# Kernel tuning notes

Measured on AMD Instinct MI355X. Metric: run time of the kernel, lower is better.

## Reference

```python
import jax, jax.numpy as jnp
import numpy as np
import math

B, T, H = 2, 1024, 2048
NH, NKV, HD = 8, 2, 256
S = 4           # altup_num_inputs
FF = 8192       # intermediate_size
LR = 64         # laurel_rank
EPS = 1e-6
ROPE_THETA = 1e6


def _ln(x, w):
    # Gemma3nRMSNorm in this repo: fp32 mean-subtract then F.layer_norm (no bias)
    x32 = x.astype(jnp.float32)
    xc = x32 - x32.mean(-1, keepdims=True)
    var = (xc * xc).mean(-1, keepdims=True)
    return (xc * jax.lax.rsqrt(var + EPS) * w.astype(jnp.float32)).astype(x.dtype)


def _rotate_half(x):
    x1, x2 = jnp.split(x, 2, axis=-1)
    return jnp.concatenate((-x2, x1), axis=-1)


def _rope(x, cos, sin):  # x: [B,nh,T,hd]; cos/sin: [B,T,hd]
    return x * cos[:, None] + _rotate_half(x) * sin[:, None]


def setup_inputs() -> dict:
    key = jax.random.key(0)
    ks = jax.random.split(key, 24)

    def w(k, shape, scale=0.02):
        return jax.random.normal(k, shape, jnp.float32) * scale

    hidden_states = jax.random.normal(ks[0], (S, B, T, H), jnp.float32)

    # real rotary embeddings
    inv_freq = 1.0 / (ROPE_THETA ** (np.arange(0, HD, 2, dtype=np.float64) / HD))
    freqs = np.arange(T, dtype=np.float64)[:, None] * inv_freq[None, :]
    emb = np.concatenate([freqs, freqs], axis=-1)  # [T,HD]
    cos = jnp.broadcast_to(jnp.asarray(np.cos(emb), jnp.float32)[None], (B, T, HD))
    sin = jnp.broadcast_to(jnp.asarray(np.sin(emb), jnp.float32)[None], (B, T, HD))

    return {
        "hidden_states": hidden_states, "cos": cos, "sin": sin,
        "wq": w(ks[1], (NH * HD, H)), "wk": w(ks[2], (NKV * HD, H)),
        "wv": w(ks[3], (NKV * HD, H)), "wo": w(ks[4], (H, NH * HD)),
        "q_norm_w": jnp.ones((HD,), jnp.float32), "k_norm_w": jnp.ones((HD,), jnp.float32),
        "input_ln_w": jnp.ones((H,), jnp.float32), "post_attn_ln_w": jnp.ones((H,), jnp.float32),
        "pre_ffw_ln_w": jnp.ones((H,), jnp.float32), "post_ffw_ln_w": jnp.ones((H,), jnp.float32),
        "gate_w": w(ks[5], (FF, H)), "up_w": w(ks[6], (FF, H)), "down_w": w(ks[7], (H, FF)),
        "laurel_left_w": w(ks[8], (LR, H)), "laurel_right_w": w(ks[9], (H, LR)),
        "laurel_norm_w": jnp.ones((H,), jnp.float32),
        "router_norm_w": jnp.ones((H,), jnp.float32),
        "router_w": w(ks[10], (S, H)),
        "pred_coef_w": w(ks[11], (S * S, S)),
        "corr_coef_w": w(ks[12], (S, S)),
        "correct_output_scale": w(ks[13], (H,), 1.0),
    }


def reference(hidden_states, cos, sin, wq, wk, wv, wo, q_norm_w, k_norm_w,
              input_ln_w, post_attn_ln_w, pre_ffw_ln_w, post_ffw_ln_w,
              gate_w, up_w, down_w, laurel_left_w, laurel_right_w, laurel_norm_w,
              router_norm_w, router_w, pred_coef_w, corr_coef_w, correct_output_scale):
    def modalities_of(x):  # router: RMSNorm -> scale -> linear -> tanh
        r = _ln(x, router_norm_w) * (1.0 / H)
        return jnp.tanh((r @ router_w.T).astype(jnp.float32)).astype(x.dtype)

    # ---- AltUp predict ----
    m = modalities_of(hidden_states[0])                      # [B,T,S]
    coefs = (m @ pred_coef_w.T).reshape(B, T, S, S)          # raw [B,T,S_out,S_in]
    # torch: matmul(h.permute(1,2,3,0), coefs.permute(0,1,3,2)) => sum_s h[s]*raw[...,j,s]
    predictions = jnp.einsum('sbth,btjs->jbth', hidden_states, coefs) + hidden_states

    active = predictions[0]
    x_norm = _ln(active, input_ln_w)

    # ---- Laurel block ----
    lau = (x_norm @ laurel_left_w.T) @ laurel_right_w.T
    laurel_out = x_norm + _ln(lau, laurel_norm_w)

    # ---- Attention (GQA, q/k/v norms, rope, scale=1.0) ----
    q = _ln((x_norm @ wq.T).reshape(B, T, NH, HD), q_norm_w).transpose(0, 2, 1, 3)
    q = _rope(q, cos, sin)
    k = _ln((x_norm @ wk.T).reshape(B, T, NKV, HD), k_norm_w).transpose(0, 2, 1, 3)
    k = _rope(k, cos, sin)
    v = _ln((x_norm @ wv.T).reshape(B, T, NKV, HD), jnp.ones((HD,), jnp.float32))
    v = v.transpose(0, 2, 1, 3)
    rep = NH // NKV
    k = jnp.repeat(k, rep, axis=1)
    v = jnp.repeat(v, rep, axis=1)
    scores = jnp.einsum('bhqd,bhkd->bhqk', q, k)             # scaling = 1.0 in Gemma3n
    causal = jnp.tril(jnp.ones((T, T), bool))
    scores = jnp.where(causal, scores, jnp.finfo(jnp.float32).min)
    attn = jax.nn.softmax(scores.astype(jnp.float32), axis=-1).astype(q.dtype)
    out = jnp.einsum('bhqk,bhkd->bhqd', attn, v)
    out = out.transpose(0, 2, 1, 3).reshape(B, T, NH * HD) @ wo.T
    out = _ln(out, post_attn_ln_w)

    attn_gated = active + out
    attn_laurel = (attn_gated + laurel_out) * (1.0 / math.sqrt(2.0))

    # ---- MLP (gelu-tanh gated) ----
    h = _ln(attn_laurel, pre_ffw_ln_w)
    ffw = (jax.nn.gelu(h @ gate_w.T, approximate=True) * (h @ up_w.T)) @ down_w.T
    ffw = _ln(ffw, post_ffw_ln_w)
    activated = attn_laurel + ffw

    # ---- AltUp correct ----
    mc = modalities_of(activated)                            # [B,T,S]
    innovation = activated - predictions[0]                  # [B,T,H]
    ccoefs = (mc @ corr_coef_w.T) + 1.0                      # [B,T,S]
    corrected = innovation[None] * ccoefs.transpose(2, 0, 1)[..., None] + predictions

    # scale_corrected_output on the active stream (altup_correct_scale=True)
    first = (corrected[0] * correct_output_scale).astype(corrected.dtype)
    corrected = corrected.at[0].set(first)
    return corrected
```

## Files before the change

kernel.cpp:

```cpp
#include <hip/hip_runtime.h>
#include <hip/hip_bf16.h>
#include <math.h>

#define B_   2
#define T_   1024
#define H_   2048
#define NH_  8
#define NKV_ 2
#define HD_  256
#define S_   4
#define FF_  8192
#define LR_  64
#define ROWS_ (B_*T_)
#define EPS_ 1e-6f

typedef __attribute__((ext_vector_type(8))) __bf16 bf16x8;
typedef __attribute__((ext_vector_type(4))) float floatx4;
typedef __attribute__((ext_vector_type(8))) unsigned short ushort8v;

__device__ __forceinline__ unsigned short f2bf(float f) {
    unsigned int u = __float_as_uint(f);
    return (unsigned short)((u + 0x7FFFu + ((u >> 16) & 1u)) >> 16);
}

__device__ __forceinline__ void gl_lds16(const void* g, void* l) {
    __builtin_amdgcn_global_load_lds(
        (const __attribute__((address_space(1))) void*)g,
        (__attribute__((address_space(3))) void*)l, 16, 0, 0);
}

__device__ __forceinline__ int swz_sigma(int r15) {
    return (r15 & 3) ^ ((r15 >> 2) & 3);
}

__device__ __forceinline__ float block_sum(float v) {
    __shared__ float s4[4];
    #pragma unroll
    for (int o = 32; o > 0; o >>= 1) v += __shfl_down(v, o, 64);
    int lane = threadIdx.x & 63;
    int w    = threadIdx.x >> 6;
    __syncthreads();
    if (lane == 0) s4[w] = v;
    __syncthreads();
    return s4[0] + s4[1] + s4[2] + s4[3];
}

__device__ __forceinline__ float block_max(float v) {
    __shared__ float s4m[4];
    #pragma unroll
    for (int o = 32; o > 0; o >>= 1) v = fmaxf(v, __shfl_down(v, o, 64));
    int lane = threadIdx.x & 63;
    int w    = threadIdx.x >> 6;
    __syncthreads();
    if (lane == 0) s4m[w] = v;
    __syncthreads();
    return fmaxf(fmaxf(s4m[0], s4m[1]), fmaxf(s4m[2], s4m[3]));
}

__global__ __launch_bounds__(256) void cvt_bf16(
    const float* __restrict__ in, unsigned short* __restrict__ out, int n)
{
    int i = (blockIdx.x * 256 + threadIdx.x) * 8;
    if (i >= n) return;
    float4 v0 = *reinterpret_cast<const float4*>(in + i);
    float4 v1 = *reinterpret_cast<const float4*>(in + i + 4);
    ushort8v o;
    o[0] = f2bf(v0.x); o[1] = f2bf(v0.y); o[2] = f2bf(v0.z); o[3] = f2bf(v0.w);
    o[4] = f2bf(v1.x); o[5] = f2bf(v1.y); o[6] = f2bf(v1.z); o[7] = f2bf(v1.w);
    *reinterpret_cast<ushort8v*>(out + i) = o;
}

__global__ __launch_bounds__(256) void router_kernel(
    const float* __restrict__ x, const float* __restrict__ nw,
    const float* __restrict__ rw, float* __restrict__ mout)
{
    size_t row = blockIdx.x;
    int tid = threadIdx.x;
    const float* xr = x + row * H_;
    float v[8]; float s = 0.f;
    #pragma unroll
    for (int i = 0; i < 8; ++i) { v[i] = xr[i*256 + tid]; s += v[i]; }
    float mu = block_sum(s) * (1.f / H_);
    float ss = 0.f;
    #pragma unroll
    for (int i = 0; i < 8; ++i) { float c = v[i] - mu; ss += c * c; }
    float rstd = rsqrtf(block_sum(ss) * (1.f / H_) + EPS_);
    float n[8];
    #pragma unroll
    for (int i = 0; i < 8; ++i) n[i] = (v[i] - mu) * rstd * nw[i*256 + tid];
    for (int so = 0; so < S_; ++so) {
        float p = 0.f;
        #pragma unroll
        for (int i = 0; i < 8; ++i) p += n[i] * rw[(size_t)so * H_ + i*256 + tid];
        float dot = block_sum(p);
        if (tid == 0) mout[row * S_ + so] = tanhf(dot * (1.f / H_));
    }
}

__global__ __launch_bounds__(256) void predict_kernel(
    const float* __restrict__ hid, const float* __restrict__ m,
    const float* __restrict__ pcw, float* __restrict__ pred)
{
    size_t row = blockIdx.x;
    int tid = threadIdx.x;
    __shared__ float ms[4];
    __shared__ float c[16];
    if (tid < 4) ms[tid] = m[row * S_ + tid];
    __syncthreads();
    if (tid < 16) {
        float s = 0.f;
        #pragma unroll
        for (int i = 0; i < 4; ++i) s += ms[i] * pcw[tid * 4 + i];
        c[tid] = s;
    }
    __syncthreads();
    const size_t STRIDE = (size_t)ROWS_ * H_;
    #pragma unroll
    for (int i = 0; i < 8; ++i) {
        size_t idx = row * H_ + i*256 + tid;
        float h0 = hid[idx];
        float h1 = hid[idx + STRIDE];
        float h2 = hid[idx + 2*STRIDE];
        float h3 = hid[idx + 3*STRIDE];
        float hv[4] = {h0, h1, h2, h3};
        #pragma unroll
        for (int j = 0; j < 4; ++j) {
            float val = hv[j] + h0*c[j*4+0] + h1*c[j*4+1] + h2*c[j*4+2] + h3*c[j*4+3];
            pred[idx + (size_t)j * STRIDE] = val;
        }
    }
}

__global__ __launch_bounds__(256) void ln_residual(
    const float* __restrict__ x, const float* __restrict__ xadd,
    const float* __restrict__ w,
    const float* __restrict__ a1, const float* __restrict__ a2,
    float scale, float* __restrict__ out, unsigned short* __restrict__ outb)
{
    size_t row = blockIdx.x;
    int tid = threadIdx.x;
    const float* xr = x + row * H_;
    const float* xa = xadd ? xadd + row * H_ : nullptr;
    float v[8]; float s = 0.f;
    #pragma unroll
    for (int i = 0; i < 8; ++i) {
        v[i] = xr[i*256 + tid];
        if (xa) v[i] += xa[i*256 + tid];
        s += v[i];
    }
    float mu = block_sum(s) * (1.f / H_);
    float ss = 0.f;
    #pragma unroll
    for (int i = 0; i < 8; ++i) { float c = v[i] - mu; ss += c * c; }
    float rstd = rsqrtf(block_sum(ss) * (1.f / H_) + EPS_);
    #pragma unroll
    for (int i = 0; i < 8; ++i) {
        size_t idx = row * H_ + i*256 + tid;
        float y = (v[i] - mu) * rstd * w[i*256 + tid];
        if (a1) y += a1[idx];
        if (a2) y += a2[idx];
        y *= scale;
        if (out)  out[idx]  = y;
        if (outb) outb[idx] = f2bf(y);
    }
}

#define BM 64
#define BN 64
#define BK 32
#define LDP 68

__global__ __launch_bounds__(256) void gemm_nt(
    const float* __restrict__ A, const float* __restrict__ Bm,
    float* __restrict__ C, int M, int N, int K)
{
    __shared__ float As[BK][LDP];
    __shared__ float Bs[BK][LDP];
    int tid = threadIdx.x;
    int n0 = blockIdx.x * BN;
    int m0 = blockIdx.y * BM;
    int tx = tid & 15, ty = tid >> 4;
    int lrow = tid >> 3;
    int lk   = (tid & 7) << 2;
    float acc[4][4] = {};
    for (int k0 = 0; k0 < K; k0 += BK) {
        #pragma unroll
        for (int r = 0; r < 2; ++r) {
            int row = lrow + r * 32;
            float4 a4 = *reinterpret_cast<const float4*>(&A[(size_t)(m0 + row) * K + k0 + lk]);
            As[lk+0][row] = a4.x; As[lk+1][row] = a4.y; As[lk+2][row] = a4.z; As[lk+3][row] = a4.w;
            float4 b4 = *reinterpret_cast<const float4*>(&Bm[(size_t)(n0 + row) * K + k0 + lk]);
            Bs[lk+0][row] = b4.x; Bs[lk+1][row] = b4.y; Bs[lk+2][row] = b4.z; Bs[lk+3][row] = b4.w;
        }
        __syncthreads();
        #pragma unroll
        for (int k = 0; k < BK; ++k) {
            float4 av = *reinterpret_cast<const float4*>(&As[k][ty << 2]);
            float4 bv = *reinterpret_cast<const float4*>(&Bs[k][tx << 2]);
            float a[4] = {av.x, av.y, av.z, av.w};
            float b[4] = {bv.x, bv.y, bv.z, bv.w};
            #pragma unroll
            for (int i = 0; i < 4; ++i)
                #pragma unroll
                for (int j = 0; j < 4; ++j)
                    acc[i][j] = fmaf(a[i], b[j], acc[i][j]);
        }
        __syncthreads();
    }
    #pragma unroll
    for (int i = 0; i < 4; ++i) {
        float4 o; o.x = acc[i][0]; o.y = acc[i][1]; o.z = acc[i][2]; o.w = acc[i][3];
        *reinterpret_cast<float4*>(&C[(size_t)(m0 + (ty << 2) + i) * N + n0 + (tx << 2)]) = o;
    }
}

__global__ __launch_bounds__(256) void gemm_bf16nt(
    const unsigned short* __restrict__ A, const unsigned short* __restrict__ Bm,
    float* __restrict__ C, float* __restrict__ C2, int M, int N, int K)
{
    __shared__ unsigned short As[8192];
    __shared__ unsigned short Bs[8192];
    int tid = threadIdx.x;
    int lane = tid & 63;
    int wave = tid >> 6;
    int m0 = blockIdx.y * 128, n0 = blockIdx.x * 128;
    int Kper = K / gridDim.z;
    int kbeg = blockIdx.z * Kper;
    int kend = kbeg + Kper;
    int wm = (wave >> 1) * 64;
    int wn = (wave & 1) * 64;
    floatx4 acc[4][4] = {};

    int lr = lane >> 2;
    int kcs = (lane & 3) ^ swz_sigma(lr);
    const unsigned short* aG0 = A  + (size_t)(m0 + wave*16 + lr) * K + kcs * 8;
    const unsigned short* aG1 = aG0 + (size_t)64 * K;
    const unsigned short* bG0 = Bm + (size_t)(n0 + wave*16 + lr) * K + kcs * 8;
    const unsigned short* bG1 = bG0 + (size_t)64 * K;

    int kc = lane >> 4, mr = lane & 15;
    int kcp = (kc ^ swz_sigma(mr)) * 8;

    gl_lds16(aG0 + kbeg, &As[wave * 512]);
    gl_lds16(aG1 + kbeg, &As[2048 + wave * 512]);
    gl_lds16(bG0 + kbeg, &Bs[wave * 512]);
    gl_lds16(bG1 + kbeg, &Bs[2048 + wave * 512]);
    __syncthreads();
    int cur = 0;
    for (int k0 = kbeg; k0 < kend; k0 += 32) {
        if (k0 + 32 < kend) {
            int nb = (cur ^ 1) * 4096;
            gl_lds16(aG0 + k0 + 32, &As[nb + wave * 512]);
            gl_lds16(aG1 + k0 + 32, &As[nb + 2048 + wave * 512]);
            gl_lds16(bG0 + k0 + 32, &Bs[nb + wave * 512]);
            gl_lds16(bG1 + k0 + 32, &Bs[nb + 2048 + wave * 512]);
        }
        int cb = cur * 4096;
        bf16x8 af[4], bfv[4];
        #pragma unroll
        for (int mi = 0; mi < 4; ++mi)
            af[mi] = *reinterpret_cast<const bf16x8*>(&As[cb + (wm + mi * 16 + mr) * 32 + kcp]);
        #pragma unroll
        for (int ni = 0; ni < 4; ++ni)
            bfv[ni] = *reinterpret_cast<const bf16x8*>(&Bs[cb + (wn + ni * 16 + mr) * 32 + kcp]);
        #pragma unroll
        for (int mi = 0; mi < 4; ++mi)
            #pragma unroll
            for (int ni = 0; ni < 4; ++ni)
                acc[mi][ni] = __builtin_amdgcn_mfma_f32_16x16x32_bf16(af[mi], bfv[ni], acc[mi][ni], 0, 0, 0);
        __syncthreads();
        cur ^= 1;
    }
    float* Cout = (blockIdx.z == 0) ? C : C2;
    int quad = lane >> 4;
    #pragma unroll
    for (int mi = 0; mi < 4; ++mi)
        #pragma unroll
        for (int ni = 0; ni < 4; ++ni)
            #pragma unroll
            for (int r = 0; r < 4; ++r)
                Cout[(size_t)(m0 + wm + mi * 16 + quad * 4 + r) * N + n0 + wn + ni * 16 + mr] = acc[mi][ni][r];
}

__global__ __launch_bounds__(256) void gemm_gateup_bf16(
    const unsigned short* __restrict__ A, const unsigned short* __restrict__ G,
    const unsigned short* __restrict__ U, unsigned short* __restrict__ Cbf,
    int M, int N, int K)
{
    __shared__ unsigned short As[8192];
    __shared__ unsigned short Gs[8192];
    __shared__ unsigned short Us[8192];
    int tid = threadIdx.x;
    int lane = tid & 63;
    int wave = tid >> 6;
    int m0 = blockIdx.y * 128, n0 = blockIdx.x * 128;
    int wm  = (wave >> 1) * 64;
    int wnf = (wave & 1) * 64;
    floatx4 accg[4][4] = {};
    floatx4 accu[4][4] = {};

    int lr = lane >> 2;
    int kcs = (lane & 3) ^ swz_sigma(lr);
    const unsigned short* aG0 = A + (size_t)(m0 + wave*16 + lr) * K + kcs * 8;
    const unsigned short* aG1 = aG0 + (size_t)64 * K;
    const unsigned short* gG0 = G + (size_t)(n0 + wave*16 + lr) * K + kcs * 8;
    const unsigned short* gG1 = gG0 + (size_t)64 * K;
    const unsigned short* uG0 = U + (size_t)(n0 + wave*16 + lr) * K + kcs * 8;
    const unsigned short* uG1 = uG0 + (size_t)64 * K;

    int kc = lane >> 4, mr = lane & 15;
    int kcp = (kc ^ swz_sigma(mr)) * 8;

    gl_lds16(aG0, &As[wave * 512]);
    gl_lds16(aG1, &As[2048 + wave * 512]);
    gl_lds16(gG0, &Gs[wave * 512]);
    gl_lds16(gG1, &Gs[2048 + wave * 512]);
    gl_lds16(uG0, &Us[wave * 512]);
    gl_lds16(uG1, &Us[2048 + wave * 512]);
    __syncthreads();
    int cur = 0;
    for (int k0 = 0; k0 < K; k0 += 32) {
        if (k0 + 32 < K) {
            int nb = (cur ^ 1) * 4096;
            gl_lds16(aG0 + k0 + 32, &As[nb + wave * 512]);
            gl_lds16(aG1 + k0 + 32, &As[nb + 2048 + wave * 512]);
            gl_lds16(gG0 + k0 + 32, &Gs[nb + wave * 512]);
            gl_lds16(gG1 + k0 + 32, &Gs[nb + 2048 + wave * 512]);
            gl_lds16(uG0 + k0 + 32, &Us[nb + wave * 512]);
            gl_lds16(uG1 + k0 + 32, &Us[nb + 2048 + wave * 512]);
        }
        int cb = cur * 4096;
        bf16x8 af[4], gf[4], uf[4];
        #pragma unroll
        for (int mi = 0; mi < 4; ++mi)
            af[mi] = *reinterpret_cast<const bf16x8*>(&As[cb + (wm + mi * 16 + mr) * 32 + kcp]);
        #pragma unroll
        for (int ni = 0; ni < 4; ++ni) {
            gf[ni] = *reinterpret_cast<const bf16x8*>(&Gs[cb + (wnf + ni * 16 + mr) * 32 + kcp]);
            uf[ni] = *reinterpret_cast<const bf16x8*>(&Us[cb + (wnf + ni * 16 + mr) * 32 + kcp]);
        }
        #pragma unroll
        for (int mi = 0; mi < 4; ++mi)
            #pragma unroll
            for (int ni = 0; ni < 4; ++ni) {
                accg[mi][ni] = __builtin_amdgcn_mfma_f32_16x16x32_bf16(af[mi], gf[ni], accg[mi][ni], 0, 0, 0);
                accu[mi][ni] = __builtin_amdgcn_mfma_f32_16x16x32_bf16(af[mi], uf[ni], accu[mi][ni], 0, 0, 0);
            }
        __syncthreads();
        cur ^= 1;
    }
    int quad = lane >> 4;
    #pragma unroll
    for (int mi = 0; mi < 4; ++mi) {
        int rb = m0 + wm + mi * 16 + quad * 4;
        #pragma unroll
        for (int ni = 0; ni < 4; ++ni)
            #pragma unroll
            for (int r = 0; r < 4; ++r) {
                float g = accg[mi][ni][r];
                float gl = 0.5f * g * (1.f + tanhf(0.7978845608028654f * (g + 0.044715f * g * g * g)));
                float val = gl * accu[mi][ni][r];
                Cbf[(size_t)(rb + r) * N + n0 + wnf + ni * 16 + mr] = f2bf(val);
            }
    }
}

__global__ __launch_bounds__(256) void qkv_norm_rope_fused(
    const float* __restrict__ in, const float* __restrict__ qw,
    const float* __restrict__ kw,
    const float* __restrict__ cs, const float* __restrict__ sn,
    unsigned short* __restrict__ qo, unsigned short* __restrict__ ko,
    unsigned short* __restrict__ vo)
{
    int blk = blockIdx.x;
    int hh = blk % 12;
    int trow = blk / 12;
    int b = trow / T_;
    int t = trow % T_;
    int d = threadIdx.x;
    float x = in[(size_t)trow * 3072 + hh * HD_ + d];
    float mu = block_sum(x) * (1.f / HD_);
    float xc = x - mu;
    float var = block_sum(xc * xc) * (1.f / HD_);
    float wv_ = (hh < 8) ? qw[d] : (hh < 10 ? kw[d] : 1.f);
    float n = xc * rsqrtf(var + EPS_) * wv_;
    __shared__ float buf[HD_];
    buf[d] = n;
    __syncthreads();
    float val = n;
    if (hh < 10) {
        float c = cs[(size_t)trow * HD_ + d];
        float s = sn[(size_t)trow * HD_ + d];
        float other = (d < 128) ? -buf[d + 128] : buf[d - 128];
        val = n * c + other * s;
    }
    if (hh < 8)
        qo[(((size_t)b * NH_ + hh) * T_ + t) * HD_ + d] = f2bf(val);
    else if (hh < 10)
        ko[(((size_t)b * NKV_ + (hh - 8)) * T_ + t) * HD_ + d] = f2bf(val);
    else
        vo[(((size_t)b * NKV_ + (hh - 10)) * HD_ + d) * T_ + t] = f2bf(val);
}

__global__ __launch_bounds__(256) void qk_gemm(
    const unsigned short* __restrict__ Q, const unsigned short* __restrict__ Kt,
    float* __restrict__ S, int head_base)
{
    if (blockIdx.x > blockIdx.y) return;
    int z = blockIdx.z;
    int bh = head_base + z;
    const unsigned short* A  = Q  + (size_t)bh * T_ * HD_;
    const unsigned short* Bm = Kt + (size_t)(bh >> 2) * T_ * HD_;
    float* C = S + (size_t)z * T_ * T_;

    __shared__ unsigned short As[8192];
    __shared__ unsigned short Bs[8192];
    int tid = threadIdx.x;
    int lane = tid & 63;
    int wave = tid >> 6;
    int m0 = blockIdx.y * 128, n0 = blockIdx.x * 128;
    int wm = (wave >> 1) * 64;
    int wn = (wave & 1) * 64;
    floatx4 acc[4][4] = {};

    int lr = lane >> 2;
    int kcs = (lane & 3) ^ swz_sigma(lr);
    const unsigned short* aG0 = A  + (size_t)(m0 + wave*16 + lr) * HD_ + kcs * 8;
    const unsigned short* aG1 = aG0 + (size_t)64 * HD_;
    const unsigned short* bG0 = Bm + (size_t)(n0 + wave*16 + lr) * HD_ + kcs * 8;
    const unsigned short* bG1 = bG0 + (size_t)64 * HD_;

    int kc = lane >> 4, mr = lane & 15;
    int kcp = (kc ^ swz_sigma(mr)) * 8;

    gl_lds16(aG0, &As[wave * 512]);
    gl_lds16(aG1, &As[2048 + wave * 512]);
    gl_lds16(bG0, &Bs[wave * 512]);
    gl_lds16(bG1, &Bs[2048 + wave * 512]);
    __syncthreads();
    int cur = 0;
    for (int k0 = 0; k0 < HD_; k0 += 32) {
        if (k0 + 32 < HD_) {
            int nb = (cur ^ 1) * 4096;
            gl_lds16(aG0 + k0 + 32, &As[nb + wave * 512]);
            gl_lds16(aG1 + k0 + 32, &As[nb + 2048 + wave * 512]);
            gl_lds16(bG0 + k0 + 32, &Bs[nb + wave * 512]);
            gl_lds16(bG1 + k0 + 32, &Bs[nb + 2048 + wave * 512]);
        }
        int cb = cur * 4096;
        bf16x8 af[4], bfv[4];
        #pragma unroll
        for (int mi = 0; mi < 4; ++mi)
            af[mi] = *reinterpret_cast<const bf16x8*>(&As[cb + (wm + mi * 16 + mr) * 32 + kcp]);
        #pragma unroll
        for (int ni = 0; ni < 4; ++ni)
            bfv[ni] = *reinterpret_cast<const bf16x8*>(&Bs[cb + (wn + ni * 16 + mr) * 32 + kcp]);
        #pragma unroll
        for (int mi = 0; mi < 4; ++mi)
            #pragma unroll
            for (int ni = 0; ni < 4; ++ni)
                acc[mi][ni] = __builtin_amdgcn_mfma_f32_16x16x32_bf16(af[mi], bfv[ni], acc[mi][ni], 0, 0, 0);
        __syncthreads();
        cur ^= 1;
    }
    int quad = lane >> 4;
    #pragma unroll
    for (int mi = 0; mi < 4; ++mi)
        #pragma unroll
        for (int ni = 0; ni < 4; ++ni)
            #pragma unroll
            for (int r = 0; r < 4; ++r)
                C[(size_t)(m0 + wm + mi * 16 + quad * 4 + r) * T_ + n0 + wn + ni * 16 + mr] = acc[mi][ni][r];
}

__global__ __launch_bounds__(256) void softmax_causal(
    const float* __restrict__ S, unsigned short* __restrict__ P)
{
    int qi = blockIdx.x;
    int g  = blockIdx.y;
    int tid = threadIdx.x;
    int L = qi + 1;
    const float* Srow = S + ((size_t)g * T_ + qi) * T_;
    unsigned short* Prow = P + ((size_t)g * T_ + qi) * T_;
    float v[4];
    float mx = -3.402823466e38f;
    #pragma unroll
    for (int i = 0; i < 4; ++i) {
        int idx = i * 256 + tid;
        v[i] = (idx < L) ? Srow[idx] : -3.402823466e38f;
        mx = fmaxf(mx, v[i]);
    }
    mx = block_max(mx);
    float sm = 0.f;
    float e[4];
    #pragma unroll
    for (int i = 0; i < 4; ++i) {
        int idx = i * 256 + tid;
        e[i] = (idx < L) ? expf(v[i] - mx) : 0.f;
        sm += e[i];
    }
    sm = block_sum(sm);
    float inv = 1.f / sm;
    #pragma unroll
    for (int i = 0; i < 4; ++i)
        Prow[i * 256 + tid] = f2bf(e[i] * inv);
}

__global__ __launch_bounds__(256) void pv_gemm(
    const unsigned short* __restrict__ P, const unsigned short* __restrict__ Vt,
    unsigned short* __restrict__ Out)
{
    int z = blockIdx.z;
    int b = z >> 3;
    int h = z & 7;
    const unsigned short* A  = P  + (size_t)z * T_ * T_;
    const unsigned short* Bm = Vt + (size_t)(z >> 2) * HD_ * T_;

    __shared__ unsigned short As[8192];
    __shared__ unsigned short Bs[8192];
    int tid = threadIdx.x;
    int lane = tid & 63;
    int wave = tid >> 6;
    int m0 = blockIdx.y * 128, n0 = blockIdx.x * 128;
    int Kend = m0 + 128;
    int wm = (wave >> 1) * 64;
    int wn = (wave & 1) * 64;
    floatx4 acc[4][4] = {};

    int lr = lane >> 2;
    int kcs = (lane & 3) ^ swz_sigma(lr);
    const unsigned short* aG0 = A  + (size_t)(m0 + wave*16 + lr) * T_ + kcs * 8;
    const unsigned short* aG1 = aG0 + (size_t)64 * T_;
    const unsigned short* bG0 = Bm + (size_t)(n0 + wave*16 + lr) * T_ + kcs * 8;
    const unsigned short* bG1 = bG0 + (size_t)64 * T_;

    int kc = lane >> 4, mr = lane & 15;
    int kcp = (kc ^ swz_sigma(mr)) * 8;

    gl_lds16(aG0, &As[wave * 512]);
    gl_lds16(aG1, &As[2048 + wave * 512]);
    gl_lds16(bG0, &Bs[wave * 512]);
    gl_lds16(bG1, &Bs[2048 + wave * 512]);
    __syncthreads();
    int cur = 0;
    for (int k0 = 0; k0 < Kend; k0 += 32) {
        if (k0 + 32 < Kend) {
            int nb = (cur ^ 1) * 4096;
            gl_lds16(aG0 + k0 + 32, &As[nb + wave * 512]);
            gl_lds16(aG1 + k0 + 32, &As[nb + 2048 + wave * 512]);
            gl_lds16(bG0 + k0 + 32, &Bs[nb + wave * 512]);
            gl_lds16(bG1 + k0 + 32, &Bs[nb + 2048 + wave * 512]);
        }
        int cb = cur * 4096;
        bf16x8 af[4], bfv[4];
        #pragma unroll
        for (int mi = 0; mi < 4; ++mi)
            af[mi] = *reinterpret_cast<const bf16x8*>(&As[cb + (wm + mi * 16 + mr) * 32 + kcp]);
        #pragma unroll
        for (int ni = 0; ni < 4; ++ni)
            bfv[ni] = *reinterpret_cast<const bf16x8*>(&Bs[cb + (wn + ni * 16 + mr) * 32 + kcp]);
        #pragma unroll
        for (int mi = 0; mi < 4; ++mi)
            #pragma unroll
            for (int ni = 0; ni < 4; ++ni)
                acc[mi][ni] = __builtin_amdgcn_mfma_f32_16x16x32_bf16(af[mi], bfv[ni], acc[mi][ni], 0, 0, 0);
        __syncthreads();
        cur ^= 1;
    }
    int quad = lane >> 4;
    #pragma unroll
    for (int mi = 0; mi < 4; ++mi)
        #pragma unroll
        for (int ni = 0; ni < 4; ++ni)
            #pragma unroll
            for (int r = 0; r < 4; ++r) {
                int row = m0 + wm + mi * 16 + quad * 4 + r;
                int col = n0 + wn + ni * 16 + mr;
                Out[((size_t)(b * T_ + row)) * (NH_ * HD_) + h * HD_ + col] =
                    f2bf(acc[mi][ni][r]);
            }
}

__global__ __launch_bounds__(256) void correct_kernel(
    const float* __restrict__ act, const float* __restrict__ pred,
    const float* __restrict__ mc, const float* __restrict__ ccw,
    const float* __restrict__ cscale, float* __restrict__ out)
{
    size_t row = blockIdx.x;
    int tid = threadIdx.x;
    __shared__ float ms[4];
    __shared__ float cc[4];
    if (tid < 4) ms[tid] = mc[row * S_ + tid];
    __syncthreads();
    if (tid < 4) {
        float s = 1.f;
        #pragma unroll
        for (int i = 0; i < 4; ++i) s += ms[i] * ccw[tid * 4 + i];
        cc[tid] = s;
    }
    __syncthreads();
    const size_t STRIDE = (size_t)ROWS_ * H_;
    #pragma unroll
    for (int i = 0; i < 8; ++i) {
        size_t idx = row * H_ + i*256 + tid;
        float a  = act[idx];
        float p0 = pred[idx];
        float inn = a - p0;
        #pragma unroll
        for (int j = 0; j < 4; ++j) {
            float val = inn * cc[j] + pred[idx + (size_t)j * STRIDE];
            if (j == 0) val *= cscale[i*256 + tid];
            out[idx + (size_t)j * STRIDE] = val;
        }
    }
}

extern "C" void kernel_launch(void* const* d_in, const int* in_sizes, int n_in,
                              void* d_out, int out_size, void* d_ws, size_t ws_size,
                              hipStream_t stream)
{
    (void)in_sizes; (void)n_in; (void)out_size; (void)ws_size;
    const float* hidden         = (const float*)d_in[0];
    const float* cosp           = (const float*)d_in[1];
    const float* sinp           = (const float*)d_in[2];
    const float* wq             = (const float*)d_in[3];
    const float* wk             = (const float*)d_in[4];
    const float* wv             = (const float*)d_in[5];
    const float* wo             = (const float*)d_in[6];
    const float* q_norm_w       = (const float*)d_in[7];
    const float* k_norm_w       = (const float*)d_in[8];
    const float* input_ln_w     = (const float*)d_in[9];
    const float* post_attn_ln_w = (const float*)d_in[10];
    const float* pre_ffw_ln_w   = (const float*)d_in[11];
    const float* post_ffw_ln_w  = (const float*)d_in[12];
    const float* gate_w         = (const float*)d_in[13];
    const float* up_w           = (const float*)d_in[14];
    const float* down_w         = (const float*)d_in[15];
    const float* ll_w           = (const float*)d_in[16];
    const float* lr_w           = (const float*)d_in[17];
    const float* laurel_norm_w  = (const float*)d_in[18];
    const float* router_norm_w  = (const float*)d_in[19];
    const float* router_w       = (const float*)d_in[20];
    const float* pred_coef_w    = (const float*)d_in[21];
    const float* corr_coef_w    = (const float*)d_in[22];
    const float* cscale         = (const float*)d_in[23];
    float* outp = (float*)d_out;

    char* base = (char*)d_ws;
    float* pred   = (float*)base;              base += 67108864;
    float* xnorm  = (float*)base;              base += 16777216;
    unsigned short* xnorm_bf = (unsigned short*)base; base += 8388608;
    float* lout   = (float*)base;              base += 16777216;
    float* alaur  = (float*)base;              base += 16777216;
    float* tmpH   = (float*)base;              base += 16777216;
    float* mbuf   = (float*)base;              base += 32768;
    float* mcbuf  = (float*)base;              base += 32768;
    float* ltmp   = (float*)base;              base += 524288;
    char* arena = base;
    unsigned short* qkvw_bf = (unsigned short*)arena;
    float* qkv_pre = (float*)(arena + 12582912);
    unsigned short* Pbuf    = (unsigned short*)arena;
    unsigned short* q_bf    = (unsigned short*)(arena + 37748736);
    unsigned short* k_bf    = (unsigned short*)(arena + 46137344);
    unsigned short* vT_bf   = (unsigned short*)(arena + 48234496);
    unsigned short* attn_bf = (unsigned short*)(arena + 50331648);
    unsigned short* wo_bf   = (unsigned short*)(arena + 58720256);
    float* Sbuf             = (float*)(arena + 67108864);
    unsigned short* gate_bf = (unsigned short*)arena;
    unsigned short* up_bf   = (unsigned short*)(arena + 33554432);
    unsigned short* gu_bf   = (unsigned short*)(arena + 67108864);
    unsigned short* down_bf = gate_bf;
    float* activated = lout;

    router_kernel <<<ROWS_, 256, 0, stream>>>(hidden, router_norm_w, router_w, mbuf);
    predict_kernel<<<ROWS_, 256, 0, stream>>>(hidden, mbuf, pred_coef_w, pred);
    ln_residual   <<<ROWS_, 256, 0, stream>>>(pred, nullptr, input_ln_w, nullptr, nullptr, 1.f, xnorm, xnorm_bf);

    gemm_nt<<<dim3(LR_/BN, ROWS_/BM), 256, 0, stream>>>(xnorm, ll_w, ltmp, ROWS_, LR_, H_);
    gemm_nt<<<dim3(H_/BN,  ROWS_/BM), 256, 0, stream>>>(ltmp, lr_w, tmpH, ROWS_, H_, LR_);
    ln_residual<<<ROWS_, 256, 0, stream>>>(tmpH, nullptr, laurel_norm_w, xnorm, nullptr, 1.f, lout, nullptr);

    cvt_bf16<<<2048, 256, 0, stream>>>(wq, qkvw_bf,            4194304);
    cvt_bf16<<< 512, 256, 0, stream>>>(wk, qkvw_bf + 4194304,  1048576);
    cvt_bf16<<< 512, 256, 0, stream>>>(wv, qkvw_bf + 5242880,  1048576);
    gemm_bf16nt<<<dim3(24, 16, 1), 256, 0, stream>>>(xnorm_bf, qkvw_bf, qkv_pre, nullptr, ROWS_, 3072, H_);
    qkv_norm_rope_fused<<<ROWS_*12, 256, 0, stream>>>(qkv_pre, q_norm_w, k_norm_w, cosp, sinp, q_bf, k_bf, vT_bf);
    cvt_bf16<<<2048, 256, 0, stream>>>(wo, wo_bf, 4194304);
    for (int hb = 0; hb < B_ * NH_; hb += 8) {
        qk_gemm       <<<dim3(8, 8, 8), 256, 0, stream>>>(q_bf, k_bf, Sbuf, hb);
        softmax_causal<<<dim3(T_, 8),   256, 0, stream>>>(Sbuf, Pbuf + (size_t)hb * T_ * T_);
    }
    pv_gemm<<<dim3(2, 8, 16), 256, 0, stream>>>(Pbuf, vT_bf, attn_bf);
    gemm_bf16nt<<<dim3(16, 16, 2), 256, 0, stream>>>(attn_bf, wo_bf, tmpH, xnorm, ROWS_, H_, NH_*HD_);
    ln_residual<<<ROWS_, 256, 0, stream>>>(tmpH, xnorm, post_attn_ln_w, pred, lout, 0.7071067811865475f, alaur, nullptr);

    ln_residual<<<ROWS_, 256, 0, stream>>>(alaur, nullptr, pre_ffw_ln_w, nullptr, nullptr, 1.f, nullptr, xnorm_bf);
    cvt_bf16<<<8192, 256, 0, stream>>>(gate_w, gate_bf, 16777216);
    cvt_bf16<<<8192, 256, 0, stream>>>(up_w,   up_bf,   16777216);
    gemm_gateup_bf16<<<dim3(64, 16), 256, 0, stream>>>(xnorm_bf, gate_bf, up_bf, gu_bf, ROWS_, FF_, H_);
    cvt_bf16<<<8192, 256, 0, stream>>>(down_w, down_bf, 16777216);
    gemm_bf16nt<<<dim3(16, 16, 2), 256, 0, stream>>>(gu_bf, down_bf, tmpH, xnorm, ROWS_, H_, FF_);
    ln_residual<<<ROWS_, 256, 0, stream>>>(tmpH, xnorm, post_ffw_ln_w, alaur, nullptr, 1.f, activated, nullptr);

    router_kernel <<<ROWS_, 256, 0, stream>>>(activated, router_norm_w, router_w, mcbuf);
    correct_kernel<<<ROWS_, 256, 0, stream>>>(activated, pred, mcbuf, corr_coef_w, cscale, outp);
}
```

Baseline: 1.114 ms.

## Rework gate/up GEMM to 128x64 tiles with register-staged single-buffer LDS

Rewrites the fused gate/up GEMM kernel to use 128x64 output tiles instead of 128x128, with each wave computing 32 rows across all 64 columns. The global-to-LDS async loads with a double buffer are replaced by register prefetch into a single LDS buffer with two barriers per k-step, using a k-chunk-major LDS layout without the XOR swizzle. The grid doubles to keep coverage. The aim is lower LDS and register use for higher occupancy, at the cost of less operand reuse per block and extra synchronisation.

Result: faster. 1.020 ms (-8.4%).

```diff
diff --git a/kernel.cpp b/kernel.cpp
--- a/kernel.cpp
+++ b/kernel.cpp
@@ -287,72 +287,67 @@
     const unsigned short* __restrict__ U, unsigned short* __restrict__ Cbf,
     int M, int N, int K)
 {
-    __shared__ unsigned short As[8192];
-    __shared__ unsigned short Gs[8192];
-    __shared__ unsigned short Us[8192];
+    __shared__ unsigned short As[4096];
+    __shared__ unsigned short Gs[2048];
+    __shared__ unsigned short Us[2048];
     int tid = threadIdx.x;
     int lane = tid & 63;
     int wave = tid >> 6;
-    int m0 = blockIdx.y * 128, n0 = blockIdx.x * 128;
-    int wm  = (wave >> 1) * 64;
-    int wnf = (wave & 1) * 64;
-    floatx4 accg[4][4] = {};
-    floatx4 accu[4][4] = {};
-
-    int lr = lane >> 2;
-    int kcs = (lane & 3) ^ swz_sigma(lr);
-    const unsigned short* aG0 = A + (size_t)(m0 + wave*16 + lr) * K + kcs * 8;
-    const unsigned short* aG1 = aG0 + (size_t)64 * K;
-    const unsigned short* gG0 = G + (size_t)(n0 + wave*16 + lr) * K + kcs * 8;
-    const unsigned short* gG1 = gG0 + (size_t)64 * K;
-    const unsigned short* uG0 = U + (size_t)(n0 + wave*16 + lr) * K + kcs * 8;
-    const unsigned short* uG1 = uG0 + (size_t)64 * K;
+    int m0 = blockIdx.y * 128, n0 = blockIdx.x * 64;
+    floatx4 accg[2][4] = {};
+    floatx4 accu[2][4] = {};
+
+    int cm = tid >> 2;
+    int ck = tid & 3;
+    const unsigned short* aP0 = A + (size_t)(m0 + cm)      * K + ck * 8;
+    const unsigned short* aP1 = A + (size_t)(m0 + 64 + cm) * K + ck * 8;
+    const unsigned short* gP  = G + (size_t)(n0 + cm)      * K + ck * 8;
+    const unsigned short* uP  = U + (size_t)(n0 + cm)      * K + ck * 8;
+    unsigned short* aW0 = &As[(ck * 128 + cm) * 8];
+    unsigned short* aW1 = &As[(ck * 128 + 64 + cm) * 8];
+    unsigned short* gW  = &Gs[(ck * 64 + cm) * 8];
+    unsigned short* uW  = &Us[(ck * 64 + cm) * 8];
+
+    uint4 ra0 = *reinterpret_cast<const uint4*>(aP0);
+    uint4 ra1 = *reinterpret_cast<const uint4*>(aP1);
+    uint4 rg  = *reinterpret_cast<const uint4*>(gP);
+    uint4 ru  = *reinterpret_cast<const uint4*>(uP);
 
     int kc = lane >> 4, mr = lane & 15;
-    int kcp = (kc ^ swz_sigma(mr)) * 8;
-
-    gl_lds16(aG0, &As[wave * 512]);
-    gl_lds16(aG1, &As[2048 + wave * 512]);
-    gl_lds16(gG0, &Gs[wave * 512]);
-    gl_lds16(gG1, &Gs[2048 + wave * 512]);
-    gl_lds16(uG0, &Us[wave * 512]);
-    gl_lds16(uG1, &Us[2048 + wave * 512]);
-    __syncthreads();
-    int cur = 0;
     for (int k0 = 0; k0 < K; k0 += 32) {
+        __syncthreads();
+        *reinterpret_cast<uint4*>(aW0) = ra0;
+        *reinterpret_cast<uint4*>(aW1) = ra1;
+        *reinterpret_cast<uint4*>(gW)  = rg;
+        *reinterpret_cast<uint4*>(uW)  = ru;
+        __syncthreads();
         if (k0 + 32 < K) {
-            int nb = (cur ^ 1) * 4096;
-            gl_lds16(aG0 + k0 + 32, &As[nb + wave * 512]);
-            gl_lds16(aG1 + k0 + 32, &As[nb + 2048 + wave * 512]);
-            gl_lds16(gG0 + k0 + 32, &Gs[nb + wave * 512]);
-            gl_lds16(gG1 + k0 + 32, &Gs[nb + 2048 + wave * 512]);
-            gl_lds16(uG0 + k0 + 32, &Us[nb + wave * 512]);
-            gl_lds16(uG1 + k0 + 32, &Us[nb + 2048 + wave * 512]);
-        }
-        int cb = cur * 4096;
-        bf16x8 af[4], gf[4], uf[4];
-        #pragma unroll
-        for (int mi = 0; mi < 4; ++mi)
-            af[mi] = *reinterpret_cast<const bf16x8*>(&As[cb + (wm + mi * 16 + mr) * 32 + kcp]);
+            ra0 = *reinterpret_cast<const uint4*>(aP0 + k0 + 32);
+            ra1 = *reinterpret_cast<const uint4*>(aP1 + k0 + 32);
+            rg  = *reinterpret_cast<const uint4*>(gP + k0 + 32);
+            ru  = *reinterpret_cast<const uint4*>(uP + k0 + 32);
+        }
+        bf16x8 af[2], gf[4], uf[4];
+        #pragma unroll
+        for (int mi = 0; mi < 2; ++mi)
+            af[mi] = *reinterpret_cast<const bf16x8*>(&As[kc * 1024 + (wave * 32 + mi * 16 + mr) * 8]);
         #pragma unroll
         for (int ni = 0; ni < 4; ++ni) {
-            gf[ni] = *reinterpret_cast<const bf16x8*>(&Gs[cb + (wnf + ni * 16 + mr) * 32 + kcp]);
-            uf[ni] = *reinterpret_cast<const bf16x8*>(&Us[cb + (wnf + ni * 16 + mr) * 32 + kcp]);
-        }
-        #pragma unroll
-        for (int mi = 0; mi < 4; ++mi)
+            gf[ni] = *reinterpret_cast<const bf16x8*>(&Gs[kc * 512 + (ni * 16 + mr) * 8]);
+            uf[ni] = *reinterpret_cast<const bf16x8*>(&Us[kc * 512 + (ni * 16 + mr) * 8]);
+        }
+        #pragma unroll
+        for (int mi = 0; mi < 2; ++mi)
             #pragma unroll
             for (int ni = 0; ni < 4; ++ni) {
                 accg[mi][ni] = __builtin_amdgcn_mfma_f32_16x16x32_bf16(af[mi], gf[ni], accg[mi][ni], 0, 0, 0);
                 accu[mi][ni] = __builtin_amdgcn_mfma_f32_16x16x32_bf16(af[mi], uf[ni], accu[mi][ni], 0, 0, 0);
             }
-        __syncthreads();
-        cur ^= 1;
     }
     int quad = lane >> 4;
     #pragma unroll
-    for (int mi = 0; mi < 4; ++mi) {
-        int rb = m0 + wm + mi * 16 + quad * 4;
+    for (int mi = 0; mi < 2; ++mi) {
+        int rb = m0 + wave * 32 + mi * 16 + quad * 4;
         #pragma unroll
         for (int ni = 0; ni < 4; ++ni)
             #pragma unroll
@@ -360,7 +355,7 @@
                 float g = accg[mi][ni][r];
                 float gl = 0.5f * g * (1.f + tanhf(0.7978845608028654f * (g + 0.044715f * g * g * g)));
                 float val = gl * accu[mi][ni][r];
-                Cbf[(size_t)(rb + r) * N + n0 + wnf + ni * 16 + mr] = f2bf(val);
+                Cbf[(size_t)(rb + r) * N + n0 + ni * 16 + mr] = f2bf(val);
             }
     }
 }
@@ -697,7 +692,7 @@
     ln_residual<<<ROWS_, 256, 0, stream>>>(alaur, nullptr, pre_ffw_ln_w, nullptr, nullptr, 1.f, nullptr, xnorm_bf);
     cvt_bf16<<<8192, 256, 0, stream>>>(gate_w, gate_bf, 16777216);
     cvt_bf16<<<8192, 256, 0, stream>>>(up_w,   up_bf,   16777216);
-    gemm_gateup_bf16<<<dim3(64, 16), 256, 0, stream>>>(xnorm_bf, gate_bf, up_bf, gu_bf, ROWS_, FF_, H_);
+    gemm_gateup_bf16<<<dim3(128, 16), 256, 0, stream>>>(xnorm_bf, gate_bf, up_bf, gu_bf, ROWS_, FF_, H_);
     cvt_bf16<<<8192, 256, 0, stream>>>(down_w, down_bf, 16777216);
     gemm_bf16nt<<<dim3(16, 16, 2), 256, 0, stream>>>(gu_bf, down_bf, tmpH, xnorm, ROWS_, H_, FF_);
     ln_residual<<<ROWS_, 256, 0, stream>>>(tmpH, xnorm, post_ffw_ln_w, alaur, nullptr, 1.f, activated, nullptr);
```
